# Performance work log

Hardware: AMD Instinct MI355X
Metric: run time of the kernel (lower is better)

## Reference

```python
import jax, jax.numpy as jnp
import numpy as np

B, T, IN_DIM, STATE, OUT_DIM, K = 64, 2048, 256, 512, 256, 3
OUT_LEN = 2048
EPS = 1e-5


def setup_inputs() -> dict:
    key = jax.random.key(0)
    ks = jax.random.split(key, 8)
    x = jax.random.normal(ks[0], (B, T, IN_DIM), jnp.float32)
    W_in = jax.random.normal(ks[1], (STATE, IN_DIM), jnp.float32) * (1.0 / np.sqrt(IN_DIM))
    b_in = jnp.zeros((STATE,), jnp.float32)
    conv_w = jax.random.normal(ks[2], (STATE, STATE, K), jnp.float32) * (1.0 / np.sqrt(STATE * K))
    conv_b = jnp.zeros((STATE,), jnp.float32)
    bn_gamma = jnp.ones((STATE,), jnp.float32)
    bn_beta = jnp.zeros((STATE,), jnp.float32)
    ln_gamma = jnp.ones((STATE,), jnp.float32)
    ln_beta = jnp.zeros((STATE,), jnp.float32)
    A = jax.random.normal(ks[3], (STATE, STATE), jnp.float32)
    Bm = jax.random.normal(ks[4], (STATE, STATE), jnp.float32)
    C = jax.random.normal(ks[5], (STATE, OUT_DIM), jnp.float32)
    return {"x": x, "W_in": W_in, "b_in": b_in, "conv_w": conv_w, "conv_b": conv_b,
            "bn_gamma": bn_gamma, "bn_beta": bn_beta, "ln_gamma": ln_gamma, "ln_beta": ln_beta,
            "A": A, "Bm": Bm, "C": C, "output_length": OUT_LEN}


def _forward(x, W_in, b_in, conv_w, conv_b, bn_gamma, bn_beta, ln_gamma, ln_beta, A, Bm, C, output_length):
    # input projection + SiLU: (B,T,IN) -> (B,T,STATE)
    v = jax.nn.silu(x @ W_in.T + b_in)
    # depth conv over time (torch Conv1d, NCH layout)
    vc = v.transpose(0, 2, 1)  # (B, STATE, T)
    vc = jax.lax.conv_general_dilated(
        vc, conv_w, window_strides=(1,), padding=[(K // 2, K // 2)],
        dimension_numbers=("NCH", "OIH", "NCH")) + conv_b[None, :, None]
    # BatchNorm1d in training mode: stats over (batch, time) per channel
    mu = vc.mean(axis=(0, 2), keepdims=True)
    var = jnp.mean((vc - mu) ** 2, axis=(0, 2), keepdims=True)
    vc = (vc - mu) / jnp.sqrt(var + EPS) * bn_gamma[None, :, None] + bn_beta[None, :, None]
    v = vc.transpose(0, 2, 1)  # (B, T, STATE)
    # sequential matrix-state recurrence with per-step LayerNorm (dropout = eval/identity)
    vs = v[:, :output_length].transpose(1, 0, 2)  # (T, B, STATE)
    s0 = jnp.zeros((x.shape[0], STATE), x.dtype)

    def step(s, v_t):
        s = s @ A + v_t @ Bm
        m = s.mean(-1, keepdims=True)
        vv = jnp.mean((s - m) ** 2, -1, keepdims=True)
        s = (s - m) / jnp.sqrt(vv + EPS) * ln_gamma + ln_beta
        return s, s @ C

    _, ys = jax.lax.scan(step, s0, vs)  # ys: (T, B, OUT_DIM)
    return ys.transpose(1, 0, 2)  # (B, T, OUT_DIM)


def reference(x, W_in, b_in, conv_w, conv_b, bn_gamma, bn_beta, ln_gamma, ln_beta, A, Bm, C, output_length):
    return _forward(x, W_in, b_in, conv_w, conv_b, bn_gamma, bn_beta, ln_gamma, ln_beta, A, Bm, C, output_length)
```

## Files before the change

kernel.cpp:

```cpp
#include <hip/hip_runtime.h>
#include <hip/hip_bf16.h>
#include <hip/hip_fp16.h>
#include <stdint.h>


using bf16 = __hip_bfloat16;
typedef short    bf16x8 __attribute__((ext_vector_type(8)));
typedef float    f32x4v __attribute__((ext_vector_type(4)));
typedef _Float16 f16x8  __attribute__((ext_vector_type(8)));
typedef _Float16 f16x4  __attribute__((ext_vector_type(4)));

static __device__ inline unsigned short f2bf_bits(float f) {
  union { bf16 h; unsigned short u; } cv; cv.h = __float2bfloat16(f); return cv.u;
}
static __device__ inline float bflo(unsigned v) { return __builtin_bit_cast(float, v << 16); }
static __device__ inline float bfhi(unsigned v) { return __builtin_bit_cast(float, v & 0xFFFF0000u); }

static __device__ inline void glds16(const void* g, void* l) {
  __builtin_amdgcn_global_load_lds(
      (const __attribute__((address_space(1))) unsigned int*)g,
      (__attribute__((address_space(3))) unsigned int*)l, 16, 0, 0);
}

#define ASM_BAR() asm volatile("s_waitcnt lgkmcnt(0)\n\ts_barrier" ::: "memory")

__global__ void kprep(const float* __restrict__ W_in, const float* __restrict__ conv_w,
                      const float* __restrict__ A, const float* __restrict__ C,
                      const float* __restrict__ lng, const float* __restrict__ lnb,
                      float* __restrict__ sums, bf16* __restrict__ vpad,
                      bf16* __restrict__ Wt, bf16* __restrict__ Wct,
                      _Float16* __restrict__ Ctf, _Float16* __restrict__ Afr,
                      float* __restrict__ cbeta, float* __restrict__ ybeta) {
  long idx = (long)blockIdx.x * 256 + threadIdx.x;
  if (idx < 1024) { sums[idx] = 0.f; return; }
  idx -= 1024;
  if (idx < 65536) {
    long b = idx >> 10, rem = idx & 1023, r = rem >> 9, col = rem & 511;
    long row = b * 2050 + (r ? 2049 : 0);
    vpad[row * 512 + col] = __float2bfloat16(0.f);
    return;
  }
  idx -= 65536;
  if (idx < 131072) { Wt[idx] = __float2bfloat16(W_in[idx]); return; }
  idx -= 131072;
  if (idx < 786432) {
    long o = idx / 1536, k = idx - o * 1536, kk = k >> 9, i = k & 511;
    Wct[idx] = __float2bfloat16(conv_w[(o * 512 + i) * 3 + kk]);
    return;
  }
  idx -= 786432;
  if (idx < 131072) {
    long n = idx >> 9, i = idx & 511;
    Ctf[idx] = (_Float16)(C[i * 256 + n] * lng[i]);
    return;
  }
  idx -= 131072;
  if (idx < 262144) {
    long k = idx >> 9, n = idx & 511;
    long w = n >> 7, nt = (n >> 4) & 7, cc = n & 15;
    long kt = k >> 5, qq = (k & 31) >> 3, j = k & 7;
    Afr[(((w * 8 + nt) * 16 + kt) * 64 + (qq * 16 + cc)) * 8 + j] =
        (_Float16)(A[k * 512 + n] * lng[k]);
    return;
  }
  idx -= 262144;
  if (idx < 512) {
    int n = (int)idx;
    float acc = 0.f;
    for (int k = 0; k < 512; ++k) acc += lnb[k] * A[(long)k * 512 + n];
    cbeta[n] = acc;
    return;
  }
  idx -= 512;
  if (idx < 256) {
    int n = (int)idx;
    float acc = 0.f;
    for (int i = 0; i < 512; ++i) acc += lnb[i] * C[(long)i * 256 + n];
    ybeta[n] = acc;
  }
}

__global__ void kx(const float4* __restrict__ x, ushort4* __restrict__ xb) {
  size_t i = (size_t)blockIdx.x * 256 + threadIdx.x;
  float4 v = x[i];
  ushort4 o;
  o.x = f2bf_bits(v.x); o.y = f2bf_bits(v.y); o.z = f2bf_bits(v.z); o.w = f2bf_bits(v.w);
  xb[i] = o;
}

template <int EPI, bool F16>
__global__ __launch_bounds__(256)
void kgemm(const bf16* __restrict__ Ag, long lda, long rowExtra,
           const bf16* __restrict__ Bg, int K,
           const float* __restrict__ bias, void* __restrict__ outp) {
  const int tid = threadIdx.x;
  const int lane = tid & 63;
  const int wv = tid >> 6;
  const int wm = wv >> 1, wn = wv & 1;
  const long m0 = (long)blockIdx.x * 128;
  const long n0 = (long)blockIdx.y * 128;
  __shared__ short At[128 * 64];
  __shared__ short Bt[128 * 64];
  f32x4v acc[4][4];
#pragma unroll
  for (int a = 0; a < 4; ++a)
#pragma unroll
    for (int b = 0; b < 4; ++b)
#pragma unroll
      for (int r = 0; r < 4; ++r) acc[a][b][r] = 0.f;

  const int rsub = lane >> 3;
  const int ksub = (lane & 7) * 8;

  for (int k0 = 0; k0 < K; k0 += 64) {
#pragma unroll
    for (int j = 0; j < 4; ++j) {
      const int c = wv * 4 + j;
      {
        long row = m0 + c * 8 + rsub;
        const bf16* gp = Ag + row * lda + (row >> 11) * rowExtra + k0 + ksub;
        glds16(gp, At + c * 512);
      }
      {
        long row = n0 + c * 8 + rsub;
        const bf16* gp = Bg + row * (long)K + k0 + ksub;
        glds16(gp, Bt + c * 512);
      }
    }
    __syncthreads();
#pragma unroll
    for (int h = 0; h < 2; ++h) {
      bf16x8 af[4], bf_[4];
      const int kb = h * 32 + (lane >> 4) * 8;
#pragma unroll
      for (int f = 0; f < 4; ++f) {
        af[f]  = *(const bf16x8*)(At + (wm * 64 + f * 16 + (lane & 15)) * 64 + kb);
        bf_[f] = *(const bf16x8*)(Bt + (wn * 64 + f * 16 + (lane & 15)) * 64 + kb);
      }
#pragma unroll
      for (int fm = 0; fm < 4; ++fm)
#pragma unroll
        for (int fn = 0; fn < 4; ++fn) {
          if constexpr (F16)
            acc[fm][fn] = __builtin_amdgcn_mfma_f32_16x16x32_f16(
                __builtin_bit_cast(f16x8, af[fm]), __builtin_bit_cast(f16x8, bf_[fn]),
                acc[fm][fn], 0, 0, 0);
          else
            acc[fm][fn] = __builtin_amdgcn_mfma_f32_16x16x32_bf16(af[fm], bf_[fn], acc[fm][fn], 0, 0, 0);
        }
    }
    __syncthreads();
  }

  const int q = lane >> 4, cL = lane & 15;
#pragma unroll
  for (int fm = 0; fm < 4; ++fm)
#pragma unroll
    for (int fn = 0; fn < 4; ++fn)
#pragma unroll
      for (int r = 0; r < 4; ++r) {
        const long m = m0 + wm * 64 + fm * 16 + q * 4 + r;
        const long n = n0 + wn * 64 + fn * 16 + cL;
        float v = acc[fm][fn][r];
        if constexpr (EPI == 0) {
          v += bias[n];
          const float s = v / (1.f + __expf(-v));
          const long row = (m >> 11) * 2050 + (m & 2047) + 1;
          ((bf16*)outp)[row * 512 + n] = __float2bfloat16(s);
        } else if constexpr (EPI == 1) {
          ((bf16*)outp)[m * 512 + n] = __float2bfloat16(v);
        } else if constexpr (EPI == 2) {
          const long rowp = (m & 2047) * 64 + (m >> 11);
          ((bf16*)outp)[rowp * 512 + n] = __float2bfloat16(v + bias[n]);
        } else {
          ((float*)outp)[m * 256 + n] = v + bias[n];
        }
      }
}

__global__ __launch_bounds__(512)
void bn_stats(const bf16* __restrict__ cr, float* __restrict__ sums) {
  const int tid = threadIdx.x;
  const long base = (long)blockIdx.x * 128 * 512;
  float s = 0.f, q = 0.f;
  for (int r = 0; r < 128; ++r) {
    float v = __bfloat162float(cr[base + (long)r * 512 + tid]);
    s += v; q += v * v;
  }
  atomicAdd(&sums[tid], s);
  atomicAdd(&sums[512 + tid], q);
}

__global__ void bn_finalize(const float* __restrict__ sums, const float* __restrict__ gamma,
                            const float* __restrict__ beta, float* __restrict__ scsh) {
  const int n = threadIdx.x;
  const float mu = sums[n] * (1.f / 131072.f);
  const float var = sums[512 + n] * (1.f / 131072.f) - mu * mu;
  const float sc = gamma[n] * rsqrtf(var + 1e-5f);
  scsh[n] = sc;
  scsh[512 + n] = beta[n] - mu * sc;
}

__global__ void build_bm(const float* __restrict__ Bm, const float* __restrict__ scsh,
                         const float* __restrict__ cbeta,
                         bf16* __restrict__ Bmt, float* __restrict__ biasu) {
  long idx = (long)blockIdx.x * 256 + threadIdx.x;
  if (idx < 262144) {
    long n = idx >> 9, i = idx & 511;
    Bmt[idx] = __float2bfloat16(Bm[i * 512 + n] * scsh[i]);
  } else if (idx < 262656) {
    int n = (int)(idx - 262144);
    float acc = cbeta[n];
    for (int i = 0; i < 512; ++i) acc += scsh[512 + i] * Bm[(long)i * 512 + n];
    biasu[n] = acc;
  }
}

__global__ __launch_bounds__(512, 2)
void krec2(const _Float16* __restrict__ Afrag,
           const ushort* __restrict__ U2,
           const float* __restrict__ cbeta,
           _Float16* __restrict__ S) {
  const int tid = threadIdx.x;
  const int lane = tid & 63, w = tid >> 6;
  const int q = lane >> 4, c = lane & 15;
  const int g = blockIdx.x;

  __shared__ _Float16 Alds[128 * 512] __attribute__((aligned(16)));
  __shared__ _Float16 slds[16 * 520] __attribute__((aligned(16)));
  __shared__ float red[256] __attribute__((aligned(16)));

  f16x8 Ar[48];
#pragma unroll
  for (int mt = 0; mt < 4; ++mt)
#pragma unroll
    for (int kt = 0; kt < 12; ++kt)
      Ar[mt * 12 + kt] = *(const f16x8*)(Afrag + (((w * 4 + mt) * 16 + kt) * 64 + lane) * 8);

#pragma unroll
  for (int mt = 0; mt < 4; ++mt)
#pragma unroll
    for (int k2 = 0; k2 < 4; ++k2)
      glds16(Afrag + (((w * 4 + mt) * 16 + 12 + k2) * 64 + lane) * 8,
             &Alds[((w * 4 + mt) * 4 + k2) * 512]);

  for (int i = tid; i < 16 * 520; i += 512) slds[i] = (_Float16)0;

  const int nb = w * 64 + q * 4;
  uint2 upre[4];
#pragma unroll
  for (int mt = 0; mt < 4; ++mt)
    upre[mt] = *(const uint2*)(U2 + ((size_t)(g * 16 + c)) * 512 + nb + mt * 16);
  __syncthreads();

#pragma unroll 1
  for (int t = 0; t < 2048; ++t) {
    f32x4v acc[4];
#pragma unroll
    for (int mt = 0; mt < 4; ++mt) {
      uint2 u = upre[mt];
      acc[mt][0] = bflo(u.x); acc[mt][1] = bfhi(u.x);
      acc[mt][2] = bflo(u.y); acc[mt][3] = bfhi(u.y);
    }
    if (t == 0) {
#pragma unroll
      for (int mt = 0; mt < 4; ++mt) {
        float4 cb = *(const float4*)(cbeta + nb + mt * 16);
        acc[mt][0] -= cb.x; acc[mt][1] -= cb.y; acc[mt][2] -= cb.z; acc[mt][3] -= cb.w;
      }
    }
    const int tnx = (t < 2047) ? t + 1 : 2047;
#pragma unroll
    for (int mt = 0; mt < 4; ++mt)
      upre[mt] = *(const uint2*)(U2 + ((size_t)tnx * 64 + g * 16 + c) * 512 + nb + mt * 16);
#pragma unroll
    for (int kt = 0; kt < 12; ++kt) {
      f16x8 sf = *(const f16x8*)&slds[c * 520 + kt * 32 + q * 8];
#pragma unroll
      for (int mt = 0; mt < 4; ++mt)
        acc[mt] = __builtin_amdgcn_mfma_f32_16x16x32_f16(Ar[mt * 12 + kt], sf, acc[mt], 0, 0, 0);
    }
#pragma unroll
    for (int k2 = 0; k2 < 4; ++k2) {
      f16x8 sf = *(const f16x8*)&slds[c * 520 + (12 + k2) * 32 + q * 8];
#pragma unroll
      for (int mt = 0; mt < 4; ++mt) {
        f16x8 af = *(const f16x8*)&Alds[((w * 4 + mt) * 4 + k2) * 512 + lane * 8];
        acc[mt] = __builtin_amdgcn_mfma_f32_16x16x32_f16(af, sf, acc[mt], 0, 0, 0);
      }
    }
    float s0 = 0.f, s1 = 0.f, q0 = 0.f, q1 = 0.f;
#pragma unroll
    for (int mt = 0; mt < 4; ++mt) {
      float a0 = acc[mt][0], a1 = acc[mt][1], a2 = acc[mt][2], a3 = acc[mt][3];
      s0 += a0 + a2; s1 += a1 + a3;
      q0 = fmaf(a0, a0, fmaf(a2, a2, q0));
      q1 = fmaf(a1, a1, fmaf(a3, a3, q1));
    }
    float Sv = s0 + s1, Qv = q0 + q1;
    Sv += __shfl_xor(Sv, 16); Sv += __shfl_xor(Sv, 32);
    Qv += __shfl_xor(Qv, 16); Qv += __shfl_xor(Qv, 32);
    if (q == 0) *(float2*)&red[(c * 8 + w) * 2] = make_float2(Sv, Qv);
    if (t > 0) {
#pragma unroll
      for (int r = 0; r < 2; ++r) {
        f16x8 v = *(const f16x8*)&slds[(w * 2 + r) * 520 + lane * 8];
        *(f16x8*)(S + ((size_t)(g * 16 + w * 2 + r) * 2048 + (t - 1)) * 512 + lane * 8) = v;
      }
    }
    ASM_BAR();
    const float4 p0 = *(const float4*)&red[c * 16];
    const float4 p1 = *(const float4*)&red[c * 16 + 4];
    const float4 p2 = *(const float4*)&red[c * 16 + 8];
    const float4 p3 = *(const float4*)&red[c * 16 + 12];
    const float fs = ((p0.x + p0.z) + (p1.x + p1.z)) + ((p2.x + p2.z) + (p3.x + p3.z));
    const float fq = ((p0.y + p0.w) + (p1.y + p1.w)) + ((p2.y + p2.w) + (p3.y + p3.w));
    const float mu = fs * (1.f / 512.f);
    const float rs = rsqrtf(fq * (1.f / 512.f) - mu * mu + 1e-5f);
    const float off = -mu * rs;
#pragma unroll
    for (int mt = 0; mt < 4; ++mt) {
      f16x4 pk;
#pragma unroll
      for (int r = 0; r < 4; ++r) pk[r] = (_Float16)fmaf(acc[mt][r], rs, off);
      *(f16x4*)&slds[c * 520 + nb + mt * 16] = pk;
    }
    ASM_BAR();
  }
#pragma unroll
  for (int r = 0; r < 2; ++r) {
    f16x8 v = *(const f16x8*)&slds[(w * 2 + r) * 520 + lane * 8];
    *(f16x8*)(S + ((size_t)(g * 16 + w * 2 + r) * 2048 + 2047) * 512 + lane * 8) = v;
  }
}

extern "C" void kernel_launch(void* const* d_in, const int* in_sizes, int n_in,
                              void* d_out, int out_size, void* d_ws, size_t ws_size,
                              hipStream_t stream) {
  (void)in_sizes; (void)n_in; (void)out_size; (void)ws_size;
  const float* x     = (const float*)d_in[0];
  const float* W_in  = (const float*)d_in[1];
  const float* b_in  = (const float*)d_in[2];
  const float* convw = (const float*)d_in[3];
  const float* bng   = (const float*)d_in[5];
  const float* bnb   = (const float*)d_in[6];
  const float* lng   = (const float*)d_in[7];
  const float* lnb   = (const float*)d_in[8];
  const float* Am    = (const float*)d_in[9];
  const float* Bm    = (const float*)d_in[10];
  const float* Cm    = (const float*)d_in[11];

  char* ws = (char*)d_ws;
  bf16*      xb    = (bf16*)(ws + 0ull);
  bf16*      bufA  = (bf16*)(ws + 67108864ull);
  bf16*      bufB  = (bf16*)(ws + 201457664ull);
  bf16*      Wt    = (bf16*)(ws + 335675392ull);
  bf16*      Wct   = (bf16*)(ws + 335937536ull);
  _Float16*  Afr   = (_Float16*)(ws + 337510400ull);
  _Float16*  Ctf   = (_Float16*)(ws + 338034688ull);
  bf16*      Bmt   = (bf16*)(ws + 338296832ull);
  float*     biasu = (float*)(ws + 338821120ull);
  float*     sums  = (float*)(ws + 338823168ull);
  float*     scsh  = (float*)(ws + 338827264ull);
  float*     cbeta = (float*)(ws + 338831360ull);
  float*     ybeta = (float*)(ws + 338833408ull);

  kprep<<<5383, 256, 0, stream>>>(W_in, convw, Am, Cm, lng, lnb, sums, bufA, Wt, Wct, Ctf, Afr,
                                  cbeta, ybeta);
  kx<<<32768, 256, 0, stream>>>((const float4*)x, (ushort4*)xb);
  kgemm<0, false><<<dim3(1024, 4), 256, 0, stream>>>(xb, 256, 0, Wt, 256, b_in, bufA);
  kgemm<1, false><<<dim3(1024, 4), 256, 0, stream>>>(bufA, 512, 1024, Wct, 1536, nullptr, bufB);
  bn_stats<<<1024, 512, 0, stream>>>(bufB, sums);
  bn_finalize<<<1, 512, 0, stream>>>(sums, bng, bnb, scsh);
  build_bm<<<1026, 256, 0, stream>>>(Bm, scsh, cbeta, Bmt, biasu);
  kgemm<2, false><<<dim3(1024, 4), 256, 0, stream>>>(bufB, 512, 0, Bmt, 512, biasu, bufA);
  krec2<<<4, 512, 0, stream>>>(Afr, (const ushort*)bufA, cbeta, (_Float16*)bufB);
  kgemm<3, true><<<dim3(1024, 2), 256, 0, stream>>>(bufB, 512, 0, (const bf16*)Ctf, 512, ybeta, d_out);
}
```

Measured before the change: 6.013 ms.

## Stream tail A fragments from global/L2 each step instead of LDS

The recurrence kernel now keeps 10 of 16 A k-tiles in registers and streams the remaining 6 from global memory every timestep. It uses inline-asm loads with explicit vmcnt waits, interleaved with the register-resident MFMAs, replacing the 128KB LDS copy of A. The S stores are moved to the start of the step, and the reduction buffer is changed to a padded per-wave layout. The goal is to free LDS and registers and hide load latency behind MFMAs on this latency-bound sequential loop. The cost is repeated L2 traffic each step, and the hand-counted vmcnt waits are fragile.

Result: slower. 14.01 ms (+132.9%).

```diff
diff --git a/kernel.cpp b/kernel.cpp
--- a/kernel.cpp
+++ b/kernel.cpp
@@ -23,6 +23,21 @@
 }
 
 #define ASM_BAR() asm volatile("s_waitcnt lgkmcnt(0)\n\ts_barrier" ::: "memory")
+
+#define WAITV(N) do { asm volatile("s_waitcnt vmcnt(" #N ")"); \
+                      __builtin_amdgcn_sched_barrier(0); } while (0)
+
+template <int IMM>
+static __device__ inline void gload_a(f16x8& d, const _Float16* p) {
+  asm volatile("global_load_dwordx4 %0, %1, off offset:%2"
+               : "=v"(d) : "v"(p), "i"(IMM));
+}
+static __device__ inline void gload_u2(uint2& d, const ushort* p) {
+  asm volatile("global_load_dwordx2 %0, %1, off" : "=v"(d) : "v"(p));
+}
+static __device__ inline void gstore8(_Float16* p, f16x8 v) {
+  asm volatile("global_store_dwordx4 %0, %1, off" :: "v"(p), "v"(v));
+}
 
 __global__ void kprep(const float* __restrict__ W_in, const float* __restrict__ conv_w,
                       const float* __restrict__ A, const float* __restrict__ C,
@@ -217,7 +232,7 @@
 }
 
 __global__ __launch_bounds__(512, 2)
-void krec2(const _Float16* __restrict__ Afrag,
+void krec3(const _Float16* __restrict__ Afrag,
            const ushort* __restrict__ U2,
            const float* __restrict__ cbeta,
            _Float16* __restrict__ S) {
@@ -226,35 +241,58 @@
   const int q = lane >> 4, c = lane & 15;
   const int g = blockIdx.x;
 
-  __shared__ _Float16 Alds[128 * 512] __attribute__((aligned(16)));
   __shared__ _Float16 slds[16 * 520] __attribute__((aligned(16)));
-  __shared__ float red[256] __attribute__((aligned(16)));
-
-  f16x8 Ar[48];
+  __shared__ float2 red[8 * 17] __attribute__((aligned(16)));
+
+  f16x8 Ar[40];
 #pragma unroll
   for (int mt = 0; mt < 4; ++mt)
 #pragma unroll
-    for (int kt = 0; kt < 12; ++kt)
-      Ar[mt * 12 + kt] = *(const f16x8*)(Afrag + (((w * 4 + mt) * 16 + kt) * 64 + lane) * 8);
-
-#pragma unroll
-  for (int mt = 0; mt < 4; ++mt)
-#pragma unroll
-    for (int k2 = 0; k2 < 4; ++k2)
-      glds16(Afrag + (((w * 4 + mt) * 16 + 12 + k2) * 64 + lane) * 8,
-             &Alds[((w * 4 + mt) * 4 + k2) * 512]);
+    for (int kt = 0; kt < 10; ++kt)
+      Ar[mt * 10 + kt] = *(const f16x8*)(Afrag + (((w * 4 + mt) * 16 + kt) * 64 + lane) * 8);
+
+  const _Float16* ab0 = Afrag + (((w * 4 + 0) * 16 + 12) * 64 + lane) * 8;
+  const _Float16* ab1 = Afrag + (((w * 4 + 1) * 16 + 12) * 64 + lane) * 8;
+  const _Float16* ab2 = Afrag + (((w * 4 + 2) * 16 + 12) * 64 + lane) * 8;
+  const _Float16* ab3 = Afrag + (((w * 4 + 3) * 16 + 12) * 64 + lane) * 8;
+#define ISSUE_A(fr, IMM) do { gload_a<IMM>(fr[0], ab0); gload_a<IMM>(fr[1], ab1); \
+                              gload_a<IMM>(fr[2], ab2); gload_a<IMM>(fr[3], ab3); } while (0)
+#define MFMA_AR(kt) do { \
+    f16x8 sf = *(const f16x8*)&slds[c * 520 + (kt) * 32 + q * 8]; \
+    acc[0] = __builtin_amdgcn_mfma_f32_16x16x32_f16(Ar[0 * 10 + (kt)], sf, acc[0], 0, 0, 0); \
+    acc[1] = __builtin_amdgcn_mfma_f32_16x16x32_f16(Ar[1 * 10 + (kt)], sf, acc[1], 0, 0, 0); \
+    acc[2] = __builtin_amdgcn_mfma_f32_16x16x32_f16(Ar[2 * 10 + (kt)], sf, acc[2], 0, 0, 0); \
+    acc[3] = __builtin_amdgcn_mfma_f32_16x16x32_f16(Ar[3 * 10 + (kt)], sf, acc[3], 0, 0, 0); } while (0)
+#define MFMA_GL(fr, kt) do { \
+    f16x8 sf = *(const f16x8*)&slds[c * 520 + (kt) * 32 + q * 8]; \
+    acc[0] = __builtin_amdgcn_mfma_f32_16x16x32_f16(fr[0], sf, acc[0], 0, 0, 0); \
+    acc[1] = __builtin_amdgcn_mfma_f32_16x16x32_f16(fr[1], sf, acc[1], 0, 0, 0); \
+    acc[2] = __builtin_amdgcn_mfma_f32_16x16x32_f16(fr[2], sf, acc[2], 0, 0, 0); \
+    acc[3] = __builtin_amdgcn_mfma_f32_16x16x32_f16(fr[3], sf, acc[3], 0, 0, 0); } while (0)
 
   for (int i = tid; i < 16 * 520; i += 512) slds[i] = (_Float16)0;
 
   const int nb = w * 64 + q * 4;
+  const ushort* uptr = U2 + ((size_t)(g * 16 + c)) * 512 + nb;
   uint2 upre[4];
 #pragma unroll
-  for (int mt = 0; mt < 4; ++mt)
-    upre[mt] = *(const uint2*)(U2 + ((size_t)(g * 16 + c)) * 512 + nb + mt * 16);
+  for (int mt = 0; mt < 4; ++mt) gload_u2(upre[mt], uptr + mt * 16);
+  uptr += 32768;
+  _Float16* sp0 = S + ((size_t)(g * 16 + w * 2 + 0) * 2048) * 512 + lane * 8;
+  _Float16* sp1 = S + ((size_t)(g * 16 + w * 2 + 1) * 2048) * 512 + lane * 8;
+
+  WAITV(0);
   __syncthreads();
 
 #pragma unroll 1
   for (int t = 0; t < 2048; ++t) {
+    if (t > 0) {
+      f16x8 v0 = *(const f16x8*)&slds[(w * 2 + 0) * 520 + lane * 8];
+      f16x8 v1 = *(const f16x8*)&slds[(w * 2 + 1) * 520 + lane * 8];
+      gstore8(sp0, v0); gstore8(sp1, v1);
+      sp0 += 512; sp1 += 512;
+    }
+    WAITV(2);
     f32x4v acc[4];
 #pragma unroll
     for (int mt = 0; mt < 4; ++mt) {
@@ -269,26 +307,27 @@
         acc[mt][0] -= cb.x; acc[mt][1] -= cb.y; acc[mt][2] -= cb.z; acc[mt][3] -= cb.w;
       }
     }
-    const int tnx = (t < 2047) ? t + 1 : 2047;
-#pragma unroll
-    for (int mt = 0; mt < 4; ++mt)
-      upre[mt] = *(const uint2*)(U2 + ((size_t)tnx * 64 + g * 16 + c) * 512 + nb + mt * 16);
-#pragma unroll
-    for (int kt = 0; kt < 12; ++kt) {
-      f16x8 sf = *(const f16x8*)&slds[c * 520 + kt * 32 + q * 8];
-#pragma unroll
-      for (int mt = 0; mt < 4; ++mt)
-        acc[mt] = __builtin_amdgcn_mfma_f32_16x16x32_f16(Ar[mt * 12 + kt], sf, acc[mt], 0, 0, 0);
-    }
-#pragma unroll
-    for (int k2 = 0; k2 < 4; ++k2) {
-      f16x8 sf = *(const f16x8*)&slds[c * 520 + (12 + k2) * 32 + q * 8];
-#pragma unroll
-      for (int mt = 0; mt < 4; ++mt) {
-        f16x8 af = *(const f16x8*)&Alds[((w * 4 + mt) * 4 + k2) * 512 + lane * 8];
-        acc[mt] = __builtin_amdgcn_mfma_f32_16x16x32_f16(af, sf, acc[mt], 0, 0, 0);
-      }
-    }
+    f16x8 fA[4], fB[4], fC[4], fD[4], fE[4], fF[4];
+    ISSUE_A(fA, -2048);
+    MFMA_AR(0); MFMA_AR(1);
+    ISSUE_A(fB, -1024);
+    MFMA_AR(2); MFMA_AR(3);
+    WAITV(4); MFMA_GL(fA, 10);
+    ISSUE_A(fC, 0);
+    MFMA_AR(4); MFMA_AR(5);
+    WAITV(4); MFMA_GL(fB, 11);
+    ISSUE_A(fD, 1024);
+    MFMA_AR(6); MFMA_AR(7);
+    WAITV(4); MFMA_GL(fC, 12);
+    ISSUE_A(fE, 2048);
+    MFMA_AR(8); MFMA_AR(9);
+    WAITV(4); MFMA_GL(fD, 13);
+    ISSUE_A(fF, 3072);
+#pragma unroll
+    for (int mt = 0; mt < 4; ++mt) gload_u2(upre[mt], uptr + mt * 16);
+    uptr += 32768;
+    WAITV(8); MFMA_GL(fE, 14);
+    WAITV(4); MFMA_GL(fF, 15);
     float s0 = 0.f, s1 = 0.f, q0 = 0.f, q1 = 0.f;
 #pragma unroll
     for (int mt = 0; mt < 4; ++mt) {
@@ -300,21 +339,14 @@
     float Sv = s0 + s1, Qv = q0 + q1;
     Sv += __shfl_xor(Sv, 16); Sv += __shfl_xor(Sv, 32);
     Qv += __shfl_xor(Qv, 16); Qv += __shfl_xor(Qv, 32);
-    if (q == 0) *(float2*)&red[(c * 8 + w) * 2] = make_float2(Sv, Qv);
-    if (t > 0) {
-#pragma unroll
-      for (int r = 0; r < 2; ++r) {
-        f16x8 v = *(const f16x8*)&slds[(w * 2 + r) * 520 + lane * 8];
-        *(f16x8*)(S + ((size_t)(g * 16 + w * 2 + r) * 2048 + (t - 1)) * 512 + lane * 8) = v;
-      }
-    }
+    if (q == 0) red[w * 17 + c] = make_float2(Sv, Qv);
     ASM_BAR();
-    const float4 p0 = *(const float4*)&red[c * 16];
-    const float4 p1 = *(const float4*)&red[c * 16 + 4];
-    const float4 p2 = *(const float4*)&red[c * 16 + 8];
-    const float4 p3 = *(const float4*)&red[c * 16 + 12];
-    const float fs = ((p0.x + p0.z) + (p1.x + p1.z)) + ((p2.x + p2.z) + (p3.x + p3.z));
-    const float fq = ((p0.y + p0.w) + (p1.y + p1.w)) + ((p2.y + p2.w) + (p3.y + p3.w));
+    float2 r0 = red[0 * 17 + c], r1 = red[1 * 17 + c];
+    float2 r2 = red[2 * 17 + c], r3 = red[3 * 17 + c];
+    float2 r4 = red[4 * 17 + c], r5 = red[5 * 17 + c];
+    float2 r6 = red[6 * 17 + c], r7 = red[7 * 17 + c];
+    const float fs = ((r0.x + r1.x) + (r2.x + r3.x)) + ((r4.x + r5.x) + (r6.x + r7.x));
+    const float fq = ((r0.y + r1.y) + (r2.y + r3.y)) + ((r4.y + r5.y) + (r6.y + r7.y));
     const float mu = fs * (1.f / 512.f);
     const float rs = rsqrtf(fq * (1.f / 512.f) - mu * mu + 1e-5f);
     const float off = -mu * rs;
@@ -332,6 +364,9 @@
     f16x8 v = *(const f16x8*)&slds[(w * 2 + r) * 520 + lane * 8];
     *(f16x8*)(S + ((size_t)(g * 16 + w * 2 + r) * 2048 + 2047) * 512 + lane * 8) = v;
   }
+#undef ISSUE_A
+#undef MFMA_AR
+#undef MFMA_GL
 }
 
 extern "C" void kernel_launch(void* const* d_in, const int* in_sizes, int n_in,
@@ -374,6 +409,6 @@
   bn_finalize<<<1, 512, 0, stream>>>(sums, bng, bnb, scsh);
   build_bm<<<1026, 256, 0, stream>>>(Bm, scsh, cbeta, Bmt, biasu);
   kgemm<2, false><<<dim3(1024, 4), 256, 0, stream>>>(bufB, 512, 0, Bmt, 512, biasu, bufA);
-  krec2<<<4, 512, 0, stream>>>(Afr, (const ushort*)bufA, cbeta, (_Float16*)bufB);
+  krec3<<<4, 512, 0, stream>>>(Afr, (const ushort*)bufA, cbeta, (_Float16*)bufB);
   kgemm<3, true><<<dim3(1024, 2), 256, 0, stream>>>(bufB, 512, 0, (const bf16*)Ctf, 512, ybeta, d_out);
 }
```
